# Optimization experiments

Measured on AMD Instinct MI355X. Metric: run time of the kernel, lower is better.

The kernel has to match this reference:

```python
import jax, jax.numpy as jnp
import numpy as np

N = 40000          # nodes
E = 640000         # edges (avg degree 16)
D = 128            # in_channels == out_channels
G = 8              # graphs
NPG = N // G       # nodes per graph
EPS = 1e-6
SLOPE = 0.01       # torch LeakyReLU default


def leaky(x):
    return jnp.where(x >= 0, x, SLOPE * x)


def setup_inputs() -> dict:
    key = jax.random.key(0)
    ks = jax.random.split(key, 8)
    x = jax.random.normal(ks[0], (N, D), dtype=jnp.float32)
    edge_index = jax.random.randint(ks[1], (2, E), 0, N, dtype=jnp.int32)
    w = jax.random.uniform(ks[2], (E, 1), dtype=jnp.float32)
    batch = jnp.repeat(jnp.arange(G, dtype=jnp.int32), NPG)
    batch_num = jnp.full((G,), NPG, dtype=jnp.int32)
    s = 1.0 / np.sqrt(D)
    W1 = jax.random.uniform(ks[3], (D, D), jnp.float32, -s, s)
    W2 = jax.random.uniform(ks[4], (D, D), jnp.float32, -s, s)
    Wo = jax.random.uniform(ks[5], (D, D), jnp.float32, -s, s)
    Wn = jax.random.uniform(ks[6], (D, D), jnp.float32, -s, s)
    gamma = jnp.ones((D,), jnp.float32)
    beta = jnp.zeros((D,), jnp.float32)
    return {"x": x, "edge_index": edge_index, "w": w, "batch": batch,
            "batch_num": batch_num, "W1": W1, "W2": W2, "Wo": Wo, "Wn": Wn,
            "gamma": gamma, "beta": beta}


def reference(x, edge_index, w, batch, batch_num, W1, W2, Wo, Wn, gamma, beta):
    # mlp_x (dropout in eval mode => identity)
    h = leaky(x @ W1) @ W2                                    # [N, D]
    # gather -> scale -> scatter-sum -> activate
    xj = w * h[edge_index[1]]                                 # [E, D]
    xn = leaky(jax.ops.segment_sum(xj, edge_index[0], num_segments=N))
    out = h @ Wo + xn @ Wn                                    # [N, D]
    # GraphNorm: per-graph mean and unbiased std (torch_scatter defaults)
    cnt = batch_num.astype(jnp.float32)[:, None]              # [G, 1]
    mu = jax.ops.segment_sum(out, batch, num_segments=G) / cnt
    diff = out - mu[batch]
    var = jax.ops.segment_sum(diff * diff, batch, num_segments=G) / (cnt - 1.0)
    sigma = jnp.sqrt(var)
    return diff / (sigma[batch] + EPS) * gamma + beta
```

## Files before the change

kernel.cpp:

```cpp
#include <hip/hip_runtime.h>
#include <hip/hip_bf16.h>

#define D 128
#define NN 40000
#define EE 640000
#define GG 8
#define NPG 5000
#define CSUB 16
#define OVCAP 4095

using short8 = __attribute__((ext_vector_type(8))) short;
using f32x4 = __attribute__((ext_vector_type(4))) float;

__device__ __forceinline__ float lrelu(float v) { return v >= 0.f ? v : 0.01f * v; }

__device__ __forceinline__ ushort f2bf(float f) {
    union { float f; uint u; } c; c.f = f;
    return (ushort)((c.u + 0x7FFFu + ((c.u >> 16) & 1u)) >> 16);
}
__device__ __forceinline__ float bf2f_lo(uint u) { union { uint u; float f; } c; c.u = u << 16; return c.f; }
__device__ __forceinline__ float bf2f_hi(uint u) { union { uint u; float f; } c; c.u = u & 0xFFFF0000u; return c.f; }

__global__ __launch_bounds__(256) void prep_k(const float* __restrict__ W1,
                                              const float* __restrict__ W2,
                                              const float* __restrict__ Wo,
                                              const float* __restrict__ Wn,
                                              short* __restrict__ WT,
                                              uint4* __restrict__ zbase, int zlen16) {
    const int b = blockIdx.x;
    if (b < 4) {
        const float* W = b == 0 ? W1 : b == 1 ? W2 : b == 2 ? Wo : Wn;
        short* T = WT + b * (D * D);
#pragma unroll 4
        for (int i = 0; i < 64; ++i) {
            int flat = threadIdx.x + i * 256;
            int k = flat >> 7, n = flat & 127;
            T[n * D + k] = (short)f2bf(W[flat]);
        }
    } else {
        int idx = (b - 4) * 256 + threadIdx.x;
        if (idx < zlen16) zbase[idx] = uint4{0, 0, 0, 0};
    }
}

__device__ __forceinline__ void stage_B(const short* __restrict__ WT,
                                        short (*Bs)[136], int tid) {
    const uint4* bsrc = (const uint4*)WT;
#pragma unroll
    for (int i = 0; i < 8; ++i) {
        int idx = tid + i * 256;
        int flat = idx * 8;
        *(uint4*)&Bs[flat >> 7][flat & 127] = bsrc[idx];
    }
}

template <int ABF>
__device__ __forceinline__ void stage_A(const void* __restrict__ Av,
                                        short (*As)[136], int arow, int tid) {
    if constexpr (ABF) {
        const uint4* asrc = (const uint4*)Av;
#pragma unroll
        for (int i = 0; i < 4; ++i) {
            int idx = tid + i * 256;
            int flat = idx * 8;
            *(uint4*)&As[flat >> 7][flat & 127] = asrc[(size_t)arow * 16 + idx];
        }
    } else {
        const float4* A4 = (const float4*)Av;
#pragma unroll
        for (int i = 0; i < 8; ++i) {
            int idx = tid + i * 256;
            int row = idx >> 5, kq = idx & 31;
            float4 v = A4[(size_t)(arow + row) * 32 + kq];
            uint2 p;
            p.x = (uint)f2bf(v.x) | ((uint)f2bf(v.y) << 16);
            p.y = (uint)f2bf(v.z) | ((uint)f2bf(v.w) << 16);
            *(uint2*)&As[row][kq * 4] = p;
        }
    }
}

__device__ __forceinline__ void do_mfma(short (*As)[136], short (*Bs)[136],
                                        f32x4 (&acc)[8], int tid) {
    const int lane = tid & 63;
    const int m0 = (tid >> 6) * 16;
    const int lrow = lane & 15;
    const int kgrp = (lane >> 4) * 8;
#pragma unroll
    for (int ks = 0; ks < 4; ++ks) {
        const int kb = ks * 32 + kgrp;
        short8 a = *(const short8*)&As[m0 + lrow][kb];
#pragma unroll
        for (int nt = 0; nt < 8; ++nt) {
            short8 b = *(const short8*)&Bs[nt * 16 + lrow][kb];
            acc[nt] = __builtin_amdgcn_mfma_f32_16x16x32_bf16(a, b, acc[nt], 0, 0, 0);
        }
    }
}

__global__ __launch_bounds__(256) void mlp_k(const float* __restrict__ x,
                                             const short* __restrict__ W1T,
                                             const short* __restrict__ W2T,
                                             ushort* __restrict__ h) {
    __shared__ short As[64][136];
    __shared__ short Bs[128][136];
    const int tid = threadIdx.x;
    const int arow = blockIdx.x * 64;
    f32x4 acc[8] = {};
    stage_A<0>(x, As, arow, tid);
    stage_B(W1T, Bs, tid);
    __syncthreads();
    do_mfma(As, Bs, acc, tid);
    __syncthreads();
    const int lane = tid & 63;
    const int c0 = lane & 15;
    const int r0 = (tid >> 6) * 16 + ((lane >> 4) << 2);
#pragma unroll
    for (int nt = 0; nt < 8; ++nt)
#pragma unroll
        for (int r = 0; r < 4; ++r)
            As[r0 + r][nt * 16 + c0] = (short)f2bf(lrelu(acc[nt][r]));
    stage_B(W2T, Bs, tid);
#pragma unroll
    for (int nt = 0; nt < 8; ++nt) acc[nt] = f32x4{0.f, 0.f, 0.f, 0.f};
    __syncthreads();
    do_mfma(As, Bs, acc, tid);
#pragma unroll
    for (int nt = 0; nt < 8; ++nt)
#pragma unroll
        for (int r = 0; r < 4; ++r)
            h[(size_t)(arow + r0 + r) * D + nt * 16 + c0] = f2bf(acc[nt][r]);
}

__global__ __launch_bounds__(256) void fill_k(const int* __restrict__ ei,
                                              const float* __restrict__ w,
                                              int* __restrict__ deg4,
                                              int2* __restrict__ csr,
                                              int* __restrict__ ov) {
    const int t = blockIdx.x * 256 + threadIdx.x;
    const int e0 = t * 4;
    const int4 dst = *(const int4*)&ei[e0];
    const int4 src = *(const int4*)&ei[EE + e0];
    const float4 wv = *(const float4*)&w[e0];
    const int ds[4] = {dst.x, dst.y, dst.z, dst.w};
    const int sr[4] = {src.x, src.y, src.z, src.w};
    const float wf[4] = {wv.x, wv.y, wv.z, wv.w};
    int pos[4];
#pragma unroll
    for (int k = 0; k < 4; ++k) pos[k] = atomicAdd(&deg4[k * NN + ds[k]], 1);
#pragma unroll
    for (int k = 0; k < 4; ++k) {
        if (pos[k] < CSUB) {
            csr[(size_t)ds[k] * 64 + k * CSUB + pos[k]] = make_int2(sr[k], __float_as_int(wf[k]));
        } else {
            const int oi = atomicAdd(&ov[0], 1);
            if (oi < OVCAP) ov[1 + oi] = e0 + k;
        }
    }
}

__global__ __launch_bounds__(256) void gather_k(const ushort* __restrict__ h,
                                                const int* __restrict__ deg4,
                                                const int2* __restrict__ csr,
                                                const int* __restrict__ ei,
                                                const float* __restrict__ w,
                                                const int* __restrict__ ov,
                                                ushort* __restrict__ xnact) {
    const int n = blockIdx.x * 16 + (threadIdx.x >> 4);
    const int lane = threadIdx.x & 15;
    const int d0 = deg4[0 * NN + n], d1 = deg4[1 * NN + n];
    const int d2 = deg4[2 * NN + n], d3 = deg4[3 * NN + n];
    const int c0 = min(d0, CSUB), c1 = min(d1, CSUB);
    const int c2 = min(d2, CSUB), c3 = min(d3, CSUB);
    const int t0 = c0, t1 = t0 + c1, t2 = t1 + c2;
    const int total = t2 + c3;
    const int2* row = csr + (size_t)n * 64;
    float acc[8] = {};
    int j = 0;
    for (; j + 8 <= total; j += 8) {
        int2 p[8]; uint4 v[8];
#pragma unroll
        for (int t = 0; t < 8; ++t) {
            const int jj = j + t;
            const int s = jj < t0 ? jj
                        : jj < t1 ? jj - t0 + CSUB
                        : jj < t2 ? jj - t1 + 2 * CSUB
                                  : jj - t2 + 3 * CSUB;
            p[t] = row[s];
        }
#pragma unroll
        for (int t = 0; t < 8; ++t) v[t] = *((const uint4*)(h + (size_t)p[t].x * D) + lane);
#pragma unroll
        for (int t = 0; t < 8; ++t) {
            const float wv = __int_as_float(p[t].y);
            acc[0] += wv * bf2f_lo(v[t].x); acc[1] += wv * bf2f_hi(v[t].x);
            acc[2] += wv * bf2f_lo(v[t].y); acc[3] += wv * bf2f_hi(v[t].y);
            acc[4] += wv * bf2f_lo(v[t].z); acc[5] += wv * bf2f_hi(v[t].z);
            acc[6] += wv * bf2f_lo(v[t].w); acc[7] += wv * bf2f_hi(v[t].w);
        }
    }
    if (j + 4 <= total) {
        int2 p[4]; uint4 v[4];
#pragma unroll
        for (int t = 0; t < 4; ++t) {
            const int jj = j + t;
            const int s = jj < t0 ? jj
                        : jj < t1 ? jj - t0 + CSUB
                        : jj < t2 ? jj - t1 + 2 * CSUB
                                  : jj - t2 + 3 * CSUB;
            p[t] = row[s];
        }
#pragma unroll
        for (int t = 0; t < 4; ++t) v[t] = *((const uint4*)(h + (size_t)p[t].x * D) + lane);
#pragma unroll
        for (int t = 0; t < 4; ++t) {
            const float wv = __int_as_float(p[t].y);
            acc[0] += wv * bf2f_lo(v[t].x); acc[1] += wv * bf2f_hi(v[t].x);
            acc[2] += wv * bf2f_lo(v[t].y); acc[3] += wv * bf2f_hi(v[t].y);
            acc[4] += wv * bf2f_lo(v[t].z); acc[5] += wv * bf2f_hi(v[t].z);
            acc[6] += wv * bf2f_lo(v[t].w); acc[7] += wv * bf2f_hi(v[t].w);
        }
        j += 4;
    }
    for (; j < total; ++j) {
        const int s = j < t0 ? j
                    : j < t1 ? j - t0 + CSUB
                    : j < t2 ? j - t1 + 2 * CSUB
                             : j - t2 + 3 * CSUB;
        const int2 p = row[s];
        const uint4 v = *((const uint4*)(h + (size_t)p.x * D) + lane);
        const float wv = __int_as_float(p.y);
        acc[0] += wv * bf2f_lo(v.x); acc[1] += wv * bf2f_hi(v.x);
        acc[2] += wv * bf2f_lo(v.y); acc[3] += wv * bf2f_hi(v.y);
        acc[4] += wv * bf2f_lo(v.z); acc[5] += wv * bf2f_hi(v.z);
        acc[6] += wv * bf2f_lo(v.w); acc[7] += wv * bf2f_hi(v.w);
    }
    if (d0 > CSUB || d1 > CSUB || d2 > CSUB || d3 > CSUB) {
        const int cnt = min(ov[0], OVCAP);
        for (int i = 0; i < cnt; ++i) {
            const int e = ov[1 + i];
            if (ei[e] == n) {
                const float wv = w[e];
                const uint4 v = *((const uint4*)(h + (size_t)ei[EE + e] * D) + lane);
                acc[0] += wv * bf2f_lo(v.x); acc[1] += wv * bf2f_hi(v.x);
                acc[2] += wv * bf2f_lo(v.y); acc[3] += wv * bf2f_hi(v.y);
                acc[4] += wv * bf2f_lo(v.z); acc[5] += wv * bf2f_hi(v.z);
                acc[6] += wv * bf2f_lo(v.w); acc[7] += wv * bf2f_hi(v.w);
            }
        }
    }
    uint4 st;
    st.x = (uint)f2bf(lrelu(acc[0])) | ((uint)f2bf(lrelu(acc[1])) << 16);
    st.y = (uint)f2bf(lrelu(acc[2])) | ((uint)f2bf(lrelu(acc[3])) << 16);
    st.z = (uint)f2bf(lrelu(acc[4])) | ((uint)f2bf(lrelu(acc[5])) << 16);
    st.w = (uint)f2bf(lrelu(acc[6])) | ((uint)f2bf(lrelu(acc[7])) << 16);
    *((uint4*)(xnact + (size_t)n * D) + lane) = st;
}

__global__ __launch_bounds__(256) void mmstats_k(const ushort* __restrict__ h,
                                                 const short* __restrict__ WoT,
                                                 const ushort* __restrict__ xa,
                                                 const short* __restrict__ WnT,
                                                 float* __restrict__ out,
                                                 float* __restrict__ stats) {
    __shared__ short As[64][136];
    __shared__ short Bs[128][136];
    const int tid = threadIdx.x;
    const int arow = blockIdx.x * 64;
    f32x4 acc[8] = {};
    stage_A<1>(h, As, arow, tid);
    stage_B(WoT, Bs, tid);
    __syncthreads();
    do_mfma(As, Bs, acc, tid);
    __syncthreads();
    stage_A<1>(xa, As, arow, tid);
    stage_B(WnT, Bs, tid);
    __syncthreads();
    do_mfma(As, Bs, acc, tid);
    __syncthreads();
    float* ls_s = (float*)As;
    float* ls_q = ls_s + 16 * 132;
    const int lane = tid & 63;
    const int c0 = lane & 15;
    const int r0 = (tid >> 6) * 16 + ((lane >> 4) << 2);
    const int li = (tid >> 6) * 4 + (lane >> 4);
#pragma unroll
    for (int nt = 0; nt < 8; ++nt) {
        float s = 0.f, q = 0.f;
#pragma unroll
        for (int r = 0; r < 4; ++r) {
            const float v = acc[nt][r];
            out[(size_t)(arow + r0 + r) * D + nt * 16 + c0] = v;
            s += v; q += v * v;
        }
        ls_s[li * 132 + nt * 16 + c0] = s;
        ls_q[li * 132 + nt * 16 + c0] = q;
    }
    __syncthreads();
    if (tid < 128) {
        const int g0 = arow / NPG;
        const int gsplit = (g0 + 1) * NPG - arow;
        float s0 = 0.f, q0 = 0.f, s1 = 0.f, q1 = 0.f;
#pragma unroll
        for (int i = 0; i < 16; ++i) {
            const float sv = ls_s[i * 132 + tid];
            const float qv = ls_q[i * 132 + tid];
            if (i * 4 >= gsplit) { s1 += sv; q1 += qv; }
            else { s0 += sv; q0 += qv; }
        }
        const int rep = blockIdx.x & 7;
        float* S = &stats[((size_t)(rep * 2 + 0) * GG + g0) * D + tid];
        float* Q = &stats[((size_t)(rep * 2 + 1) * GG + g0) * D + tid];
        atomicAdd(S, s0);
        atomicAdd(Q, q0);
        if (gsplit < 64) { atomicAdd(S + D, s1); atomicAdd(Q + D, q1); }
    }
}

__global__ __launch_bounds__(256) void norm_k(float* __restrict__ out,
                                              const float* __restrict__ stats,
                                              const float* __restrict__ gamma,
                                              const float* __restrict__ beta) {
    const int i4 = blockIdx.x * 256 + threadIdx.x;
    const int row = i4 >> 5;
    const int g = row / NPG;
    const int d0 = (i4 & 31) * 4;
    float4 v = *((float4*)out + i4);
    float4 s4 = {0.f, 0.f, 0.f, 0.f}, q4 = {0.f, 0.f, 0.f, 0.f};
#pragma unroll
    for (int rep = 0; rep < 8; ++rep) {
        const float4 sr = *(const float4*)&stats[((size_t)(rep * 2 + 0) * GG + g) * D + d0];
        const float4 qr = *(const float4*)&stats[((size_t)(rep * 2 + 1) * GG + g) * D + d0];
        s4.x += sr.x; s4.y += sr.y; s4.z += sr.z; s4.w += sr.w;
        q4.x += qr.x; q4.y += qr.y; q4.z += qr.z; q4.w += qr.w;
    }
    const float4 g4 = *(const float4*)&gamma[d0];
    const float4 b4 = *(const float4*)&beta[d0];
    const float inv = 1.f / (float)NPG;
    const float invm1 = 1.f / (float)(NPG - 1);
    float mu, var, sg;
    mu = s4.x * inv; var = (q4.x - s4.x * mu) * invm1; sg = sqrtf(fmaxf(var, 0.f));
    v.x = (v.x - mu) / (sg + 1e-6f) * g4.x + b4.x;
    mu = s4.y * inv; var = (q4.y - s4.y * mu) * invm1; sg = sqrtf(fmaxf(var, 0.f));
    v.y = (v.y - mu) / (sg + 1e-6f) * g4.y + b4.y;
    mu = s4.z * inv; var = (q4.z - s4.z * mu) * invm1; sg = sqrtf(fmaxf(var, 0.f));
    v.z = (v.z - mu) / (sg + 1e-6f) * g4.z + b4.z;
    mu = s4.w * inv; var = (q4.w - s4.w * mu) * invm1; sg = sqrtf(fmaxf(var, 0.f));
    v.w = (v.w - mu) / (sg + 1e-6f) * g4.w + b4.w;
    *((float4*)out + i4) = v;
}

extern "C" void kernel_launch(void* const* d_in, const int* in_sizes, int n_in,
                              void* d_out, int out_size, void* d_ws, size_t ws_size,
                              hipStream_t stream) {
    const float* x = (const float*)d_in[0];
    const int* ei = (const int*)d_in[1];
    const float* w = (const float*)d_in[2];
    const float* W1 = (const float*)d_in[5];
    const float* W2 = (const float*)d_in[6];
    const float* Wo = (const float*)d_in[7];
    const float* Wn = (const float*)d_in[8];
    const float* gamma = (const float*)d_in[9];
    const float* beta = (const float*)d_in[10];
    float* out = (float*)d_out;

    char* ws = (char*)d_ws;
    const size_t BF16MAT = (size_t)NN * D * 2;
    size_t off = 0;
    ushort* h = (ushort*)(ws + off);      off += BF16MAT;
    ushort* xnact = (ushort*)(ws + off);  off += BF16MAT;
    const size_t ZOFF = off;
    float* stats = (float*)(ws + off);    off += 8 * 2 * GG * D * 4;
    int* deg4 = (int*)(ws + off);         off += (size_t)NN * 4 * 4;
    int* ov = (int*)(ws + off);           off += (1 + OVCAP) * 4;
    const int ZLEN16 = (int)((off - ZOFF) / 16);
    short* WT = (short*)(ws + off);       off += 4 * (size_t)D * D * 2;
    int2* csr = (int2*)(ws + off);

    prep_k<<<4 + (ZLEN16 + 255) / 256, 256, 0, stream>>>(W1, W2, Wo, Wn, WT,
                                                         (uint4*)(ws + ZOFF), ZLEN16);
    mlp_k<<<NN / 64, 256, 0, stream>>>(x, WT, WT + D * D, h);
    fill_k<<<EE / (256 * 4), 256, 0, stream>>>(ei, w, deg4, csr, ov);
    gather_k<<<NN / 16, 256, 0, stream>>>(h, deg4, csr, ei, w, ov, xnact);
    mmstats_k<<<NN / 64, 256, 0, stream>>>(h, WT + 2 * D * D, xnact, WT + 3 * D * D, out, stats);
    norm_k<<<(NN * D / 4) / 256, 256, 0, stream>>>(out, stats, gamma, beta);
}
```

Before: 198.8 us.

## Load MFMA A fragments from global, widen CSR buckets, add stats reduce pass

```diff
diff --git a/kernel.cpp b/kernel.cpp
--- a/kernel.cpp
+++ b/kernel.cpp
@@ -7,7 +7,9 @@
 #define GG 8
 #define NPG 5000
 #define CSUB 16
+#define NBKT 8
 #define OVCAP 4095
+#define REP 32
 
 using short8 = __attribute__((ext_vector_type(8))) short;
 using f32x4 = __attribute__((ext_vector_type(4))) float;
@@ -54,46 +56,15 @@
     }
 }
 
-template <int ABF>
-__device__ __forceinline__ void stage_A(const void* __restrict__ Av,
-                                        short (*As)[136], int arow, int tid) {
-    if constexpr (ABF) {
-        const uint4* asrc = (const uint4*)Av;
-#pragma unroll
-        for (int i = 0; i < 4; ++i) {
-            int idx = tid + i * 256;
-            int flat = idx * 8;
-            *(uint4*)&As[flat >> 7][flat & 127] = asrc[(size_t)arow * 16 + idx];
-        }
-    } else {
-        const float4* A4 = (const float4*)Av;
-#pragma unroll
-        for (int i = 0; i < 8; ++i) {
-            int idx = tid + i * 256;
-            int row = idx >> 5, kq = idx & 31;
-            float4 v = A4[(size_t)(arow + row) * 32 + kq];
-            uint2 p;
-            p.x = (uint)f2bf(v.x) | ((uint)f2bf(v.y) << 16);
-            p.y = (uint)f2bf(v.z) | ((uint)f2bf(v.w) << 16);
-            *(uint2*)&As[row][kq * 4] = p;
-        }
-    }
-}
-
-__device__ __forceinline__ void do_mfma(short (*As)[136], short (*Bs)[136],
-                                        f32x4 (&acc)[8], int tid) {
-    const int lane = tid & 63;
-    const int m0 = (tid >> 6) * 16;
-    const int lrow = lane & 15;
-    const int kgrp = (lane >> 4) * 8;
+__device__ __forceinline__ void mfma8(const short8 (&a)[4], short (*Bs)[136],
+                                      f32x4 (&acc)[8], int lrow, int kgrp) {
 #pragma unroll
     for (int ks = 0; ks < 4; ++ks) {
         const int kb = ks * 32 + kgrp;
-        short8 a = *(const short8*)&As[m0 + lrow][kb];
 #pragma unroll
         for (int nt = 0; nt < 8; ++nt) {
             short8 b = *(const short8*)&Bs[nt * 16 + lrow][kb];
-            acc[nt] = __builtin_amdgcn_mfma_f32_16x16x32_bf16(a, b, acc[nt], 0, 0, 0);
+            acc[nt] = __builtin_amdgcn_mfma_f32_16x16x32_bf16(a[ks], b, acc[nt], 0, 0, 0);
         }
     }
 }
@@ -102,43 +73,61 @@
                                              const short* __restrict__ W1T,
                                              const short* __restrict__ W2T,
                                              ushort* __restrict__ h) {
-    __shared__ short As[64][136];
     __shared__ short Bs[128][136];
+    __shared__ short tw[4][16][136];
     const int tid = threadIdx.x;
+    const int wv = tid >> 6, lane = tid & 63;
+    const int lrow = lane & 15, kgrp = (lane >> 4) * 8;
+    const int m0 = wv * 16;
     const int arow = blockIdx.x * 64;
+    short8 a[4];
+#pragma unroll
+    for (int ks = 0; ks < 4; ++ks) {
+        const float* xp = &x[(size_t)(arow + m0 + lrow) * D + ks * 32 + kgrp];
+        const float4 u0 = *(const float4*)xp;
+        const float4 u1 = *(const float4*)(xp + 4);
+        short8 aa;
+        aa[0] = (short)f2bf(u0.x); aa[1] = (short)f2bf(u0.y);
+        aa[2] = (short)f2bf(u0.z); aa[3] = (short)f2bf(u0.w);
+        aa[4] = (short)f2bf(u1.x); aa[5] = (short)f2bf(u1.y);
+        aa[6] = (short)f2bf(u1.z); aa[7] = (short)f2bf(u1.w);
+        a[ks] = aa;
+    }
+    stage_B(W1T, Bs, tid);
+    __syncthreads();
     f32x4 acc[8] = {};
-    stage_A<0>(x, As, arow, tid);
-    stage_B(W1T, Bs, tid);
-    __syncthreads();
-    do_mfma(As, Bs, acc, tid);
-    __syncthreads();
-    const int lane = tid & 63;
+    mfma8(a, Bs, acc, lrow, kgrp);
     const int c0 = lane & 15;
-    const int r0 = (tid >> 6) * 16 + ((lane >> 4) << 2);
+    const int rg = (lane >> 4) * 4;
 #pragma unroll
     for (int nt = 0; nt < 8; ++nt)
 #pragma unroll
         for (int r = 0; r < 4; ++r)
-            As[r0 + r][nt * 16 + c0] = (short)f2bf(lrelu(acc[nt][r]));
+            tw[wv][rg + r][nt * 16 + c0] = (short)f2bf(lrelu(acc[nt][r]));
+    __syncthreads();
     stage_B(W2T, Bs, tid);
 #pragma unroll
+    for (int ks = 0; ks < 4; ++ks)
+        a[ks] = *(const short8*)&tw[wv][lrow][ks * 32 + kgrp];
+#pragma unroll
     for (int nt = 0; nt < 8; ++nt) acc[nt] = f32x4{0.f, 0.f, 0.f, 0.f};
     __syncthreads();
-    do_mfma(As, Bs, acc, tid);
+    mfma8(a, Bs, acc, lrow, kgrp);
 #pragma unroll
     for (int nt = 0; nt < 8; ++nt)
 #pragma unroll
         for (int r = 0; r < 4; ++r)
-            h[(size_t)(arow + r0 + r) * D + nt * 16 + c0] = f2bf(acc[nt][r]);
+            h[(size_t)(arow + m0 + rg + r) * D + nt * 16 + c0] = f2bf(acc[nt][r]);
 }
 
 __global__ __launch_bounds__(256) void fill_k(const int* __restrict__ ei,
                                               const float* __restrict__ w,
-                                              int* __restrict__ deg4,
+                                              int* __restrict__ deg8,
                                               int2* __restrict__ csr,
                                               int* __restrict__ ov) {
     const int t = blockIdx.x * 256 + threadIdx.x;
     const int e0 = t * 4;
+    const int kbase = (t & 1) * 4;
     const int4 dst = *(const int4*)&ei[e0];
     const int4 src = *(const int4*)&ei[EE + e0];
     const float4 wv = *(const float4*)&w[e0];
@@ -147,20 +136,22 @@
     const float wf[4] = {wv.x, wv.y, wv.z, wv.w};
     int pos[4];
 #pragma unroll
-    for (int k = 0; k < 4; ++k) pos[k] = atomicAdd(&deg4[k * NN + ds[k]], 1);
-#pragma unroll
-    for (int k = 0; k < 4; ++k) {
-        if (pos[k] < CSUB) {
-            csr[(size_t)ds[k] * 64 + k * CSUB + pos[k]] = make_int2(sr[k], __float_as_int(wf[k]));
+    for (int j = 0; j < 4; ++j)
+        pos[j] = atomicAdd(&deg8[ds[j] * NBKT + kbase + j], 1);
+#pragma unroll
+    for (int j = 0; j < 4; ++j) {
+        if (pos[j] < CSUB) {
+            csr[(size_t)ds[j] * (NBKT * CSUB) + (kbase + j) * CSUB + pos[j]] =
+                make_int2(sr[j], __float_as_int(wf[j]));
         } else {
             const int oi = atomicAdd(&ov[0], 1);
-            if (oi < OVCAP) ov[1 + oi] = e0 + k;
+            if (oi < OVCAP) ov[1 + oi] = e0 + j;
         }
     }
 }
 
 __global__ __launch_bounds__(256) void gather_k(const ushort* __restrict__ h,
-                                                const int* __restrict__ deg4,
+                                                const int* __restrict__ deg8,
                                                 const int2* __restrict__ csr,
                                                 const int* __restrict__ ei,
                                                 const float* __restrict__ w,
@@ -168,66 +159,48 @@
                                                 ushort* __restrict__ xnact) {
     const int n = blockIdx.x * 16 + (threadIdx.x >> 4);
     const int lane = threadIdx.x & 15;
-    const int d0 = deg4[0 * NN + n], d1 = deg4[1 * NN + n];
-    const int d2 = deg4[2 * NN + n], d3 = deg4[3 * NN + n];
-    const int c0 = min(d0, CSUB), c1 = min(d1, CSUB);
-    const int c2 = min(d2, CSUB), c3 = min(d3, CSUB);
-    const int t0 = c0, t1 = t0 + c1, t2 = t1 + c2;
-    const int total = t2 + c3;
-    const int2* row = csr + (size_t)n * 64;
+    const int4 da = *(const int4*)&deg8[n * NBKT];
+    const int4 db = *(const int4*)&deg8[n * NBKT + 4];
+    const int b0 = min(da.x, CSUB);
+    const int b1 = b0 + min(da.y, CSUB);
+    const int b2 = b1 + min(da.z, CSUB);
+    const int b3 = b2 + min(da.w, CSUB);
+    const int b4 = b3 + min(db.x, CSUB);
+    const int b5 = b4 + min(db.y, CSUB);
+    const int b6 = b5 + min(db.z, CSUB);
+    const int total = b6 + min(db.w, CSUB);
+    const int2* row = csr + (size_t)n * (NBKT * CSUB);
+    auto slot = [&](int jj) -> int {
+        return jj < b0 ? jj
+             : jj < b1 ? jj - b0 + 16
+             : jj < b2 ? jj - b1 + 32
+             : jj < b3 ? jj - b2 + 48
+             : jj < b4 ? jj - b3 + 64
+             : jj < b5 ? jj - b4 + 80
+             : jj < b6 ? jj - b5 + 96
+             :           jj - b6 + 112;
+    };
     float acc[8] = {};
     int j = 0;
-    for (; j + 8 <= total; j += 8) {
-        int2 p[8]; uint4 v[8];
-#pragma unroll
-        for (int t = 0; t < 8; ++t) {
-            const int jj = j + t;
-            const int s = jj < t0 ? jj
-                        : jj < t1 ? jj - t0 + CSUB
-                        : jj < t2 ? jj - t1 + 2 * CSUB
-                                  : jj - t2 + 3 * CSUB;
-            p[t] = row[s];
-        }
-#pragma unroll
-        for (int t = 0; t < 8; ++t) v[t] = *((const uint4*)(h + (size_t)p[t].x * D) + lane);
-#pragma unroll
-        for (int t = 0; t < 8; ++t) {
-            const float wv = __int_as_float(p[t].y);
-            acc[0] += wv * bf2f_lo(v[t].x); acc[1] += wv * bf2f_hi(v[t].x);
-            acc[2] += wv * bf2f_lo(v[t].y); acc[3] += wv * bf2f_hi(v[t].y);
-            acc[4] += wv * bf2f_lo(v[t].z); acc[5] += wv * bf2f_hi(v[t].z);
-            acc[6] += wv * bf2f_lo(v[t].w); acc[7] += wv * bf2f_hi(v[t].w);
-        }
-    }
-    if (j + 4 <= total) {
-        int2 p[4]; uint4 v[4];
-#pragma unroll
-        for (int t = 0; t < 4; ++t) {
-            const int jj = j + t;
-            const int s = jj < t0 ? jj
-                        : jj < t1 ? jj - t0 + CSUB
-                        : jj < t2 ? jj - t1 + 2 * CSUB
-                                  : jj - t2 + 3 * CSUB;
-            p[t] = row[s];
-        }
-#pragma unroll
-        for (int t = 0; t < 4; ++t) v[t] = *((const uint4*)(h + (size_t)p[t].x * D) + lane);
-#pragma unroll
-        for (int t = 0; t < 4; ++t) {
-            const float wv = __int_as_float(p[t].y);
-            acc[0] += wv * bf2f_lo(v[t].x); acc[1] += wv * bf2f_hi(v[t].x);
-            acc[2] += wv * bf2f_lo(v[t].y); acc[3] += wv * bf2f_hi(v[t].y);
-            acc[4] += wv * bf2f_lo(v[t].z); acc[5] += wv * bf2f_hi(v[t].z);
-            acc[6] += wv * bf2f_lo(v[t].w); acc[7] += wv * bf2f_hi(v[t].w);
-        }
-        j += 4;
-    }
+#define GBODY(NB)                                                              \
+    {                                                                          \
+        int2 p[NB]; uint4 v[NB];                                               \
+        _Pragma("unroll") for (int t = 0; t < NB; ++t) p[t] = row[slot(j + t)];\
+        _Pragma("unroll") for (int t = 0; t < NB; ++t)                         \
+            v[t] = *((const uint4*)(h + (size_t)p[t].x * D) + lane);           \
+        _Pragma("unroll") for (int t = 0; t < NB; ++t) {                       \
+            const float wv = __int_as_float(p[t].y);                           \
+            acc[0] += wv * bf2f_lo(v[t].x); acc[1] += wv * bf2f_hi(v[t].x);    \
+            acc[2] += wv * bf2f_lo(v[t].y); acc[3] += wv * bf2f_hi(v[t].y);    \
+            acc[4] += wv * bf2f_lo(v[t].z); acc[5] += wv * bf2f_hi(v[t].z);    \
+            acc[6] += wv * bf2f_lo(v[t].w); acc[7] += wv * bf2f_hi(v[t].w);    \
+        }                                                                      \
+        j += NB;                                                               \
+    }
+    while (j + 16 <= total) GBODY(16)
+    while (j + 4 <= total) GBODY(4)
     for (; j < total; ++j) {
-        const int s = j < t0 ? j
-                    : j < t1 ? j - t0 + CSUB
-                    : j < t2 ? j - t1 + 2 * CSUB
-                             : j - t2 + 3 * CSUB;
-        const int2 p = row[s];
+        const int2 p = row[slot(j)];
         const uint4 v = *((const uint4*)(h + (size_t)p.x * D) + lane);
         const float wv = __int_as_float(p.y);
         acc[0] += wv * bf2f_lo(v.x); acc[1] += wv * bf2f_hi(v.x);
@@ -235,7 +208,9 @@
         acc[4] += wv * bf2f_lo(v.z); acc[5] += wv * bf2f_hi(v.z);
         acc[6] += wv * bf2f_lo(v.w); acc[7] += wv * bf2f_hi(v.w);
     }
-    if (d0 > CSUB || d1 > CSUB || d2 > CSUB || d3 > CSUB) {
+#undef GBODY
+    if (da.x > CSUB || da.y > CSUB || da.z > CSUB || da.w > CSUB ||
+        db.x > CSUB || db.y > CSUB || db.z > CSUB || db.w > CSUB) {
         const int cnt = min(ov[0], OVCAP);
         for (int i = 0; i < cnt; ++i) {
             const int e = ov[1 + i];
@@ -262,39 +237,43 @@
                                                  const ushort* __restrict__ xa,
                                                  const short* __restrict__ WnT,
                                                  float* __restrict__ out,
-                                                 float* __restrict__ stats) {
-    __shared__ short As[64][136];
+                                                 float* __restrict__ statsR) {
     __shared__ short Bs[128][136];
+    __shared__ float ls[2][16][132];
     const int tid = threadIdx.x;
+    const int wv = tid >> 6, lane = tid & 63;
+    const int lrow = lane & 15, kgrp = (lane >> 4) * 8;
+    const int m0 = wv * 16;
     const int arow = blockIdx.x * 64;
+    short8 a[4];
+#pragma unroll
+    for (int ks = 0; ks < 4; ++ks)
+        a[ks] = *(const short8*)&h[(size_t)(arow + m0 + lrow) * D + ks * 32 + kgrp];
+    stage_B(WoT, Bs, tid);
+    __syncthreads();
     f32x4 acc[8] = {};
-    stage_A<1>(h, As, arow, tid);
-    stage_B(WoT, Bs, tid);
-    __syncthreads();
-    do_mfma(As, Bs, acc, tid);
-    __syncthreads();
-    stage_A<1>(xa, As, arow, tid);
+    mfma8(a, Bs, acc, lrow, kgrp);
+#pragma unroll
+    for (int ks = 0; ks < 4; ++ks)
+        a[ks] = *(const short8*)&xa[(size_t)(arow + m0 + lrow) * D + ks * 32 + kgrp];
+    __syncthreads();
     stage_B(WnT, Bs, tid);
     __syncthreads();
-    do_mfma(As, Bs, acc, tid);
-    __syncthreads();
-    float* ls_s = (float*)As;
-    float* ls_q = ls_s + 16 * 132;
-    const int lane = tid & 63;
+    mfma8(a, Bs, acc, lrow, kgrp);
     const int c0 = lane & 15;
-    const int r0 = (tid >> 6) * 16 + ((lane >> 4) << 2);
-    const int li = (tid >> 6) * 4 + (lane >> 4);
+    const int rg = (lane >> 4) * 4;
+    const int li = wv * 4 + (lane >> 4);
 #pragma unroll
     for (int nt = 0; nt < 8; ++nt) {
         float s = 0.f, q = 0.f;
 #pragma unroll
         for (int r = 0; r < 4; ++r) {
             const float v = acc[nt][r];
-            out[(size_t)(arow + r0 + r) * D + nt * 16 + c0] = v;
+            out[(size_t)(arow + m0 + rg + r) * D + nt * 16 + c0] = v;
             s += v; q += v * v;
         }
-        ls_s[li * 132 + nt * 16 + c0] = s;
-        ls_q[li * 132 + nt * 16 + c0] = q;
+        ls[0][li][nt * 16 + c0] = s;
+        ls[1][li][nt * 16 + c0] = q;
     }
     __syncthreads();
     if (tid < 128) {
@@ -303,22 +282,31 @@
         float s0 = 0.f, q0 = 0.f, s1 = 0.f, q1 = 0.f;
 #pragma unroll
         for (int i = 0; i < 16; ++i) {
-            const float sv = ls_s[i * 132 + tid];
-            const float qv = ls_q[i * 132 + tid];
+            const float sv = ls[0][i][tid];
+            const float qv = ls[1][i][tid];
             if (i * 4 >= gsplit) { s1 += sv; q1 += qv; }
             else { s0 += sv; q0 += qv; }
         }
-        const int rep = blockIdx.x & 7;
-        float* S = &stats[((size_t)(rep * 2 + 0) * GG + g0) * D + tid];
-        float* Q = &stats[((size_t)(rep * 2 + 1) * GG + g0) * D + tid];
+        const int rep = blockIdx.x & (REP - 1);
+        float* S = &statsR[(size_t)rep * (2 * GG * D) + 0 * GG * D + g0 * D + tid];
+        float* Q = &statsR[(size_t)rep * (2 * GG * D) + 1 * GG * D + g0 * D + tid];
         atomicAdd(S, s0);
         atomicAdd(Q, q0);
         if (gsplit < 64) { atomicAdd(S + D, s1); atomicAdd(Q + D, q1); }
     }
 }
 
+__global__ __launch_bounds__(256) void reduce_k(const float* __restrict__ statsR,
+                                                float* __restrict__ statsF) {
+    const int idx = blockIdx.x * 256 + threadIdx.x;
+    float s = 0.f;
+#pragma unroll
+    for (int rep = 0; rep < REP; ++rep) s += statsR[rep * (2 * GG * D) + idx];
+    statsF[idx] = s;
+}
+
 __global__ __launch_bounds__(256) void norm_k(float* __restrict__ out,
-                                              const float* __restrict__ stats,
+                                              const float* __restrict__ statsF,
                                               const float* __restrict__ gamma,
                                               const float* __restrict__ beta) {
     const int i4 = blockIdx.x * 256 + threadIdx.x;
@@ -326,14 +314,8 @@
     const int g = row / NPG;
     const int d0 = (i4 & 31) * 4;
     float4 v = *((float4*)out + i4);
-    float4 s4 = {0.f, 0.f, 0.f, 0.f}, q4 = {0.f, 0.f, 0.f, 0.f};
-#pragma unroll
-    for (int rep = 0; rep < 8; ++rep) {
-        const float4 sr = *(const float4*)&stats[((size_t)(rep * 2 + 0) * GG + g) * D + d0];
-        const float4 qr = *(const float4*)&stats[((size_t)(rep * 2 + 1) * GG + g) * D + d0];
-        s4.x += sr.x; s4.y += sr.y; s4.z += sr.z; s4.w += sr.w;
-        q4.x += qr.x; q4.y += qr.y; q4.z += qr.z; q4.w += qr.w;
-    }
+    const float4 s4 = *(const float4*)&statsF[g * D + d0];
+    const float4 q4 = *(const float4*)&statsF[GG * D + g * D + d0];
     const float4 g4 = *(const float4*)&gamma[d0];
     const float4 b4 = *(const float4*)&beta[d0];
     const float inv = 1.f / (float)NPG;
@@ -370,8 +352,9 @@
     ushort* h = (ushort*)(ws + off);      off += BF16MAT;
     ushort* xnact = (ushort*)(ws + off);  off += BF16MAT;
     const size_t ZOFF = off;
-    float* stats = (float*)(ws + off);    off += 8 * 2 * GG * D * 4;
-    int* deg4 = (int*)(ws + off);         off += (size_t)NN * 4 * 4;
+    float* statsR = (float*)(ws + off);   off += (size_t)REP * 2 * GG * D * 4;
+    float* statsF = (float*)(ws + off);   off += 2 * GG * D * 4;
+    int* deg8 = (int*)(ws + off);         off += (size_t)NN * NBKT * 4;
     int* ov = (int*)(ws + off);           off += (1 + OVCAP) * 4;
     const int ZLEN16 = (int)((off - ZOFF) / 16);
     short* WT = (short*)(ws + off);       off += 4 * (size_t)D * D * 2;
@@ -380,8 +363,9 @@
     prep_k<<<4 + (ZLEN16 + 255) / 256, 256, 0, stream>>>(W1, W2, Wo, Wn, WT,
                                                          (uint4*)(ws + ZOFF), ZLEN16);
     mlp_k<<<NN / 64, 256, 0, stream>>>(x, WT, WT + D * D, h);
-    fill_k<<<EE / (256 * 4), 256, 0, stream>>>(ei, w, deg4, csr, ov);
-    gather_k<<<NN / 16, 256, 0, stream>>>(h, deg4, csr, ei, w, ov, xnact);
-    mmstats_k<<<NN / 64, 256, 0, stream>>>(h, WT + 2 * D * D, xnact, WT + 3 * D * D, out, stats);
-    norm_k<<<(NN * D / 4) / 256, 256, 0, stream>>>(out, stats, gamma, beta);
-}
+    fill_k<<<EE / (256 * 4), 256, 0, stream>>>(ei, w, deg8, csr, ov);
+    gather_k<<<NN / 16, 256, 0, stream>>>(h, deg8, csr, ei, w, ov, xnact);
+    mmstats_k<<<NN / 64, 256, 0, stream>>>(h, WT + 2 * D * D, xnact, WT + 3 * D * D, out, statsR);
+    reduce_k<<<(2 * GG * D) / 256, 256, 0, stream>>>(statsR, statsF);
+    norm_k<<<(NN * D / 4) / 256, 256, 0, stream>>>(out, statsF, gamma, beta);
+}
```

Measured after the change: 214.2 us. 1.08x slower.
